# Optimization experiments

Measured on AMD Instinct MI355X. Metric: run time of the kernel, lower is better.

The kernel has to match this reference:

```python
import jax, jax.numpy as jnp
import numpy as np

H = 1024      # hidden_dim
NH = 16       # num_heads
HD = H // NH  # head_dim
FF = 4 * H
EPS = 1e-5

def _ln(x, g, b):
    m = jnp.mean(x, axis=-1, keepdims=True)
    v = jnp.var(x, axis=-1, keepdims=True)
    return (x - m) * jax.lax.rsqrt(v + EPS) * g + b

def setup_inputs() -> dict:
    key = jax.random.key(0)
    ks = jax.random.split(key, 12)
    s = 1.0 / np.sqrt(H)
    inp = {
        'x': jax.random.normal(ks[0], (2, 2048, H), dtype=jnp.float32),
        'Wq': jax.random.normal(ks[1], (H, H), dtype=jnp.float32) * s,
        'bq': jnp.zeros((H,), dtype=jnp.float32),
        'Wk': jax.random.normal(ks[2], (H, H), dtype=jnp.float32) * s,
        'bk': jnp.zeros((H,), dtype=jnp.float32),
        'Wv': jax.random.normal(ks[3], (H, H), dtype=jnp.float32) * s,
        'bv': jnp.zeros((H,), dtype=jnp.float32),
        'Wo': jax.random.normal(ks[4], (H, H), dtype=jnp.float32) * s,
        'bo': jnp.zeros((H,), dtype=jnp.float32),
        'g1': jnp.ones((H,), dtype=jnp.float32),
        'b1': jnp.zeros((H,), dtype=jnp.float32),
        'W1': jax.random.normal(ks[5], (H, FF), dtype=jnp.float32) * s,
        'bf1': jnp.zeros((FF,), dtype=jnp.float32),
        'W2': jax.random.normal(ks[6], (FF, H), dtype=jnp.float32) * (1.0 / np.sqrt(FF)),
        'bf2': jnp.zeros((H,), dtype=jnp.float32),
        'g2': jnp.ones((H,), dtype=jnp.float32),
        'b2': jnp.zeros((H,), dtype=jnp.float32),
    }
    return inp

def reference(x, Wq, bq, Wk, bk, Wv, bv, Wo, bo, g1, b1, W1, bf1, W2, bf2, g2, b2):
    B, S, _ = x.shape
    residual = x
    xn = _ln(x, g1, b1)
    # [B,S,H] -> [B,NH,S,HD]
    def split_heads(t):
        return t.reshape(B, S, NH, HD).transpose(0, 2, 1, 3)
    q = split_heads(xn @ Wq + bq)
    k = split_heads(xn @ Wk + bk)
    v = split_heads(xn @ Wv + bv)
    scores = jnp.einsum('bhqd,bhkd->bhqk', q, k) / np.sqrt(HD).astype(np.float32)
    attn = jax.nn.softmax(scores, axis=-1)
    ctx = jnp.einsum('bhqk,bhkd->bhqd', attn, v)
    ctx = ctx.transpose(0, 2, 1, 3).reshape(B, S, H)
    out = ctx @ Wo + bo + residual
    residual = out
    on = _ln(out, g2, b2)
    out = jax.nn.relu(on @ W1 + bf1) @ W2 + bf2 + residual
    return out
```

## Files before the change

kernel.cpp:

```cpp
#include <hip/hip_runtime.h>
#include <hip/hip_bf16.h>

constexpr int HDIM = 1024;
constexpr int NHEAD = 16;
constexpr int FFDIM = 4096;
constexpr int SEQLEN = 2048;
constexpr int NTOK = 4096;

typedef __bf16 bf16x8 __attribute__((ext_vector_type(8)));
typedef float f32x4 __attribute__((ext_vector_type(4)));
typedef short s16x4 __attribute__((ext_vector_type(4)));

union U16x8 {
    s16x4 h[2];
    bf16x8 v;
    int4 raw;
    unsigned u[4];
    short s[8];
};

__device__ __forceinline__ short f2bf(float f) {
    union { float f; unsigned u; } c;
    c.f = f;
    return (short)((c.u + 0x8000u) >> 16);
}

__device__ __forceinline__ unsigned cvtpk(float a, float b) {
    __hip_bfloat162 h = __float22bfloat162_rn(float2{a, b});
    return *reinterpret_cast<unsigned*>(&h);
}

__device__ __forceinline__ float exp2_raw(float x) {
    float r;
    asm("v_exp_f32 %0, %1" : "=v"(r) : "v"(x));
    return r;
}

template <int N>
__device__ __forceinline__ void wait_vmcnt() {
    if constexpr (N == 0) asm volatile("s_waitcnt vmcnt(0)" ::: "memory");
    else if constexpr (N == 3) asm volatile("s_waitcnt vmcnt(3)" ::: "memory");
    else if constexpr (N == 4) asm volatile("s_waitcnt vmcnt(4)" ::: "memory");
    else if constexpr (N == 6) asm volatile("s_waitcnt vmcnt(6)" ::: "memory");
    else static_assert(N == 0, "unsupported vmcnt");
}
__device__ __forceinline__ void barrier_fence() {
    __builtin_amdgcn_s_barrier();
    asm volatile("" ::: "memory");
}

__device__ __forceinline__ void gload16(const void* gsrc, void* lds) {
    __builtin_amdgcn_global_load_lds(
        (const __attribute__((address_space(1))) unsigned int*)gsrc,
        (__attribute__((address_space(3))) unsigned int*)lds, 16, 0, 0);
}


constexpr float QSCALE = 0.18033688011112042f;

__global__ __launch_bounds__(256)
void wconv_all(const float* __restrict__ Wq, const float* __restrict__ Wk,
               const float* __restrict__ Wv, const float* __restrict__ Wo,
               const float* __restrict__ W1, const float* __restrict__ W2,
               short* __restrict__ qkvT, short* __restrict__ WoT,
               short* __restrict__ W1T, short* __restrict__ W2T) {
    int i = blockIdx.x;
    const float* W;
    short* WT;
    int K, N, bx, by;
    if (i < 2048) {
        const int w = i >> 9;
        i &= 511;
        K = HDIM; N = HDIM; bx = i & 3; by = i >> 2;
        W = w == 0 ? Wq : w == 1 ? Wk : w == 2 ? Wv : Wo;
        WT = w == 3 ? WoT : qkvT + (size_t)w * HDIM * HDIM;
    } else if (i < 4096) {
        i -= 2048;
        K = HDIM; N = FFDIM; bx = i & 15; by = i >> 4;
        W = W1; WT = W1T;
    } else {
        i -= 4096;
        K = FFDIM; N = HDIM; bx = i & 3; by = i >> 2;
        W = W2; WT = W2T;
    }
    const int n = bx * 256 + threadIdx.x;
    const int g = by >> 2, fc = by & 3;
    const int k0 = g * 32 + fc * 4;
    float a[4], c[4];
#pragma unroll
    for (int j = 0; j < 4; ++j) a[j] = W[(size_t)(k0 + j) * N + n];
#pragma unroll
    for (int j = 0; j < 4; ++j) c[j] = W[(size_t)(k0 + 16 + j) * N + n];
    U16x8 u;
    u.u[0] = cvtpk(a[0], a[1]);
    u.u[1] = cvtpk(a[2], a[3]);
    u.u[2] = cvtpk(c[0], c[1]);
    u.u[3] = cvtpk(c[2], c[3]);
    *(int4*)(WT + (size_t)n * K + by * 8) = u.raw;
}

__global__ __launch_bounds__(256)
void ln_bf16(const float* __restrict__ x, const float* __restrict__ g,
             const float* __restrict__ b, short* __restrict__ out) {
    const int row = blockIdx.x, t = threadIdx.x;
    const float* xr = x + (size_t)row * HDIM;
    float4 v = *(const float4*)&xr[t * 4];
    float s = v.x + v.y + v.z + v.w;
    float ss = v.x * v.x + v.y * v.y + v.z * v.z + v.w * v.w;
#pragma unroll
    for (int o = 32; o > 0; o >>= 1) {
        s += __shfl_down(s, o);
        ss += __shfl_down(ss, o);
    }
    __shared__ float red[8];
    const int wv = t >> 6, ln = t & 63;
    if (ln == 0) { red[wv] = s; red[4 + wv] = ss; }
    __syncthreads();
    s = red[0] + red[1] + red[2] + red[3];
    ss = red[4] + red[5] + red[6] + red[7];
    const float mean = s * (1.0f / HDIM);
    const float var = ss * (1.0f / HDIM) - mean * mean;
    const float rstd = rsqrtf(var + 1e-5f);
    float4 gv = *(const float4*)&g[t * 4];
    float4 bv = *(const float4*)&b[t * 4];
    union { s16x4 h4; uint2 u2; } pk;
    pk.u2.x = cvtpk((v.x - mean) * rstd * gv.x + bv.x, (v.y - mean) * rstd * gv.y + bv.y);
    pk.u2.y = cvtpk((v.z - mean) * rstd * gv.z + bv.z, (v.w - mean) * rstd * gv.w + bv.w);
    const int kk = (t * 4) & 31;
    const int dst = ((t * 4) & ~31) + ((kk & 15) >> 2) * 8 + (kk >> 4) * 4;
    *(s16x4*)&out[(size_t)row * HDIM + dst] = pk.h4;
}

template <int BM, int BN, int MODE>
__global__ __launch_bounds__(256, ((BM + BN) == 256) ? 3 : 4)
void gemm_bf16(const short* __restrict__ A, const short* __restrict__ BT,
               const float* __restrict__ bias, const float* __restrict__ resid,
               void* __restrict__ outp, int M, int N, int K,
               const float* __restrict__ bias2, const float* __restrict__ bias3,
               void* __restrict__ out3) {
    constexpr int MI = BM / 32, NJ = BN / 32;
    constexpr int NSEG = (BM + BN) / 16;
    constexpr int PW = NSEG / 4;
    constexpr int BUFS = (BM + BN) * 32;
    __shared__ short LdsF[3 * BUFS];
    const int tid = threadIdx.x;
    const int lane = tid & 63, wave = tid >> 6;
    const int wm = wave >> 1, wn = wave & 1;
    const int l15 = lane & 15, lg = lane >> 4;
    const int lsw = lg ^ ((l15 >> 1) & 3);
    const int m0 = blockIdx.x * BM, n0 = blockIdx.y * BN;
    const int nk = K >> 5;
    const int sr = lane >> 2;
    const int sc8 = (((lane & 3) ^ ((sr >> 1) & 3))) * 8;

    auto stage = [&](int buf, int kt) {
#pragma unroll
        for (int p = 0; p < PW; ++p) {
            const int s = wave + p * 4;
            const short* src = (s < BM / 16)
                ? A + (size_t)(m0 + s * 16 + sr) * K + kt * 32 + sc8
                : BT + (size_t)(n0 + (s - BM / 16) * 16 + sr) * K + kt * 32 + sc8;
            const int off = __builtin_amdgcn_readfirstlane(buf * BUFS * 2 + s * 1024);
            gload16(src, (char*)LdsF + off);
        }
    };

    f32x4 acc[MI][NJ] = {};
    stage(0, 0);
    if (nk > 1) stage(1, 1);
    for (int kt = 0; kt < nk; ++kt) {
        const int buf = kt % 3;
        if (kt + 1 < nk) wait_vmcnt<PW>();
        else wait_vmcnt<0>();
        barrier_fence();
        if (kt + 2 < nk) stage((kt + 2) % 3, kt + 2);
        bf16x8 af[MI], bfr[NJ];
#pragma unroll
        for (int i = 0; i < MI; ++i)
            af[i] = *(const bf16x8*)&LdsF[buf * BUFS +
                                          (wm * (BM / 2) + i * 16 + l15) * 32 + lsw * 8];
#pragma unroll
        for (int j = 0; j < NJ; ++j)
            bfr[j] = *(const bf16x8*)&LdsF[buf * BUFS +
                                           (BM + wn * (BN / 2) + j * 16 + l15) * 32 + lsw * 8];
#pragma unroll
        for (int i = 0; i < MI; ++i)
#pragma unroll
            for (int j = 0; j < NJ; ++j)
                acc[i][j] = __builtin_amdgcn_mfma_f32_16x16x32_bf16(af[i], bfr[j], acc[i][j], 0, 0, 0);
    }

    const int rbase = m0 + wm * (BM / 2);
    const int cbase = n0 + wn * (BN / 2);
    if constexpr (MODE == 0) {
#pragma unroll
        for (int i = 0; i < MI; ++i)
#pragma unroll
            for (int j = 0; j < NJ; ++j) {
                const int c = cbase + j * 16 + l15;
                const float bv = bias[c];
#pragma unroll
                for (int ii = 0; ii < 4; ++ii) {
                    const int r = rbase + i * 16 + lg * 4 + ii;
                    const size_t idx = (size_t)r * N + c;
                    ((float*)outp)[idx] = acc[i][j][ii] + bv + resid[idx];
                }
            }
    } else if constexpr (MODE == 1) {
#pragma unroll
        for (int i = 0; i < MI; ++i)
#pragma unroll
            for (int j = 0; j < NJ; ++j) {
                const int c = cbase + j * 16 + l15;
                const float bv = bias[c];
                const int cp = (c & ~31) | ((l15 >> 2) * 8 + (j & 1) * 4 + (l15 & 3));
#pragma unroll
                for (int ii = 0; ii < 4; ++ii) {
                    const int r = rbase + i * 16 + lg * 4 + ii;
                    float v = acc[i][j][ii] + bv;
                    v = v > 0.0f ? v : 0.0f;
                    ((short*)outp)[(size_t)r * N + cp] = f2bf(v);
                }
            }
    } else {
        const int which = n0 >> 10;
        if (which < 2) {
            const float* bb = which == 0 ? bias : bias2;
            const float qs = which == 0 ? QSCALE : 1.0f;
            short* QKp = (short*)outp;
#pragma unroll
            for (int i = 0; i < MI; ++i)
#pragma unroll
                for (int j = 0; j < NJ; ++j) {
                    const int c = cbase + j * 16 + l15;
                    const float bv = bb[c & 1023];
                    const int cp = (c & ~31) | ((l15 >> 2) * 8 + (j & 1) * 4 + (l15 & 3));
#pragma unroll
                    for (int ii = 0; ii < 4; ++ii) {
                        const int r = rbase + i * 16 + lg * 4 + ii;
                        QKp[(size_t)r * 2048 + cp] = f2bf((acc[i][j][ii] + bv) * qs);
                    }
                }
        } else {
            short* VTp = (short*)out3;
#pragma unroll
            for (int j = 0; j < NJ; ++j) {
                const int c = cbase + j * 16 + l15;
                const int cc = c - 2048;
                const int hh = cc >> 6, dd = cc & 63;
                const float bv = bias3[cc];
#pragma unroll
                for (int i = 0; i < MI; ++i) {
                    const int r0 = rbase + i * 16 + lg * 4;
                    const int bb_ = r0 >> 11;
                    const int s0 = r0 & (SEQLEN - 1);
                    const int sbase = (s0 & ~31) + lg * 8 + (i & 1) * 4;
                    union { s16x4 h4; uint2 u2; } pk;
                    pk.u2.x = cvtpk(acc[i][j][0] + bv, acc[i][j][1] + bv);
                    pk.u2.y = cvtpk(acc[i][j][2] + bv, acc[i][j][3] + bv);
                    *(s16x4*)&VTp[(((size_t)(bb_ * NHEAD + hh)) * 64 + dd) * SEQLEN + sbase] = pk.h4;
                }
            }
        }
    }
}

__global__ __launch_bounds__(256, 4)
void attn_fwd(const short* __restrict__ QK, const short* __restrict__ VT,
              short* __restrict__ ctx) {
    __shared__ short KlF[2 * 4096];
    __shared__ short VlF[2 * 4096];
    const int tid = threadIdx.x, lane = tid & 63, wave = tid >> 6;
    const int l15 = lane & 15, lg = lane >> 4;
    const int lsw = lg ^ ((l15 >> 1) & 3);
    const int bid = blockIdx.x;
    const int xcd = bid & 7, li = bid >> 3;
    const int bh = xcd * 4 + (li >> 5);
    const int qt = li & 31;
    const int b = bh >> 4, h = bh & 15;
    const size_t tokbase = (size_t)b * SEQLEN;
    const int sr = lane >> 2;
    const int sc8 = (((lane & 3) ^ ((sr >> 1) & 3))) * 8;

    const short* kp = QK + (tokbase + wave * 16 + sr) * 2048 + 1024 + h * 64 + sc8;
    const short* vp = VT + ((size_t)bh * 64 + wave * 16 + sr) * SEQLEN + sc8;

    auto stage = [&](int buf) {
        const int off = __builtin_amdgcn_readfirstlane(buf * 8192 + wave * 1024);
        gload16(kp, (char*)KlF + off);
        gload16(kp + 32, (char*)KlF + off + 4096);
        gload16(vp, (char*)VlF + off);
        gload16(vp + 32, (char*)VlF + off + 4096);
    };

    const short* qp = QK + (tokbase + qt * 64 + wave * 16 + l15) * 2048 + h * 64;
    bf16x8 qf[2];
    qf[0] = *(const bf16x8*)(qp + lg * 8);
    qf[1] = *(const bf16x8*)(qp + 32 + lg * 8);

    U16x8 uo;
#pragma unroll
    for (int j = 0; j < 8; ++j) uo.s[j] = 0x3F80;
    const bf16x8 onesv = uo.v;

    f32x4 o[4] = {};
    f32x4 Lacc = {};
    stage(0);
    for (int kt = 0; kt < SEQLEN / 64; ++kt) {
        const int buf = kt & 1;
        __syncthreads();
        if (kt + 1 < SEQLEN / 64) {
            kp += 64 * 2048;
            vp += 64;
            stage(buf ^ 1);
        }

        f32x4 sc[4];
        __builtin_amdgcn_s_setprio(1);
#pragma unroll
        for (int j = 0; j < 4; ++j) {
            bf16x8 kf0 = *(const bf16x8*)&KlF[buf * 4096 + (j * 16 + l15) * 32 + lsw * 8];
            bf16x8 kf1 = *(const bf16x8*)&KlF[buf * 4096 + 2048 + (j * 16 + l15) * 32 + lsw * 8];
            f32x4 z = {};
            z = __builtin_amdgcn_mfma_f32_16x16x32_bf16(kf0, qf[0], z, 0, 0, 0);
            sc[j] = __builtin_amdgcn_mfma_f32_16x16x32_bf16(kf1, qf[1], z, 0, 0, 0);
        }
        __builtin_amdgcn_s_setprio(0);

        U16x8 u0, u1;
        u0.u[0] = cvtpk(exp2_raw(sc[0][0]), exp2_raw(sc[0][1]));
        u0.u[1] = cvtpk(exp2_raw(sc[0][2]), exp2_raw(sc[0][3]));
        u0.u[2] = cvtpk(exp2_raw(sc[1][0]), exp2_raw(sc[1][1]));
        u0.u[3] = cvtpk(exp2_raw(sc[1][2]), exp2_raw(sc[1][3]));
        u1.u[0] = cvtpk(exp2_raw(sc[2][0]), exp2_raw(sc[2][1]));
        u1.u[1] = cvtpk(exp2_raw(sc[2][2]), exp2_raw(sc[2][3]));
        u1.u[2] = cvtpk(exp2_raw(sc[3][0]), exp2_raw(sc[3][1]));
        u1.u[3] = cvtpk(exp2_raw(sc[3][2]), exp2_raw(sc[3][3]));

        __builtin_amdgcn_s_setprio(1);
#pragma unroll
        for (int ks = 0; ks < 2; ++ks) {
            const bf16x8 pf = ks == 0 ? u0.v : u1.v;
            Lacc = __builtin_amdgcn_mfma_f32_16x16x32_bf16(onesv, pf, Lacc, 0, 0, 0);
#pragma unroll
            for (int fd = 0; fd < 4; ++fd) {
                bf16x8 vf = *(const bf16x8*)&VlF[buf * 4096 + ks * 2048 + (fd * 16 + l15) * 32 + lsw * 8];
                o[fd] = __builtin_amdgcn_mfma_f32_16x16x32_bf16(vf, pf, o[fd], 0, 0, 0);
            }
        }
        __builtin_amdgcn_s_setprio(0);
    }

    const float rl = 1.0f / Lacc[0];
    const int qrow = qt * 64 + wave * 16 + l15;
    short* crow = ctx + (tokbase + qrow) * HDIM + h * 64;
#pragma unroll
    for (int fd = 0; fd < 4; ++fd) {
        s16x4 v4;
#pragma unroll
        for (int ii = 0; ii < 4; ++ii) v4[ii] = f2bf(o[fd][ii] * rl);
        *(s16x4*)(crow + (fd >> 1) * 32 + lg * 8 + (fd & 1) * 4) = v4;
    }
}

extern "C" void kernel_launch(void* const* d_in, const int* in_sizes, int n_in,
                              void* d_out, int out_size, void* d_ws, size_t ws_size,
                              hipStream_t stream) {
    const float* x  = (const float*)d_in[0];
    const float* Wq = (const float*)d_in[1];
    const float* bq = (const float*)d_in[2];
    const float* Wk = (const float*)d_in[3];
    const float* bk = (const float*)d_in[4];
    const float* Wv = (const float*)d_in[5];
    const float* bv = (const float*)d_in[6];
    const float* Wo = (const float*)d_in[7];
    const float* bo = (const float*)d_in[8];
    const float* g1 = (const float*)d_in[9];
    const float* b1 = (const float*)d_in[10];
    const float* W1 = (const float*)d_in[11];
    const float* bf1 = (const float*)d_in[12];
    const float* W2 = (const float*)d_in[13];
    const float* bf2 = (const float*)d_in[14];
    const float* g2 = (const float*)d_in[15];
    const float* b2 = (const float*)d_in[16];

    char* ws = (char*)d_ws;
    const size_t MB = 1024 * 1024;
    short* qkvT = (short*)(ws + 0 * MB);
    short* WoT  = (short*)(ws + 6 * MB);
    short* W1T  = (short*)(ws + 8 * MB);
    short* W2T  = (short*)(ws + 16 * MB);
    short* xn   = (short*)(ws + 24 * MB);
    short* QKb  = (short*)(ws + 32 * MB);
    short* VTb  = (short*)(ws + 48 * MB);
    short* ctx  = (short*)(ws + 56 * MB);
    float* out1 = (float*)(ws + 64 * MB);
    short* h1   = (short*)(ws + 32 * MB);

    wconv_all<<<6144, 256, 0, stream>>>(Wq, Wk, Wv, Wo, W1, W2, qkvT, WoT, W1T, W2T);

    ln_bf16<<<NTOK, 256, 0, stream>>>(x, g1, b1, xn);

    gemm_bf16<128, 128, 2><<<dim3(NTOK / 128, 3072 / 128), 256, 0, stream>>>(
        xn, qkvT, bq, nullptr, QKb, NTOK, 3072, HDIM, bk, bv, VTb);

    attn_fwd<<<1024, 256, 0, stream>>>(QKb, VTb, ctx);

    gemm_bf16<128, 64, 0><<<dim3(NTOK / 128, HDIM / 64), 256, 0, stream>>>(
        ctx, WoT, bo, x, out1, NTOK, HDIM, HDIM, nullptr, nullptr, nullptr);

    ln_bf16<<<NTOK, 256, 0, stream>>>(out1, g2, b2, xn);

    gemm_bf16<128, 128, 1><<<dim3(NTOK / 128, FFDIM / 128), 256, 0, stream>>>(
        xn, W1T, bf1, nullptr, h1, NTOK, FFDIM, HDIM, nullptr, nullptr, nullptr);

    gemm_bf16<128, 64, 0><<<dim3(NTOK / 128, HDIM / 64), 256, 0, stream>>>(
        h1, W2T, bf2, out1, (float*)d_out, NTOK, HDIM, FFDIM, nullptr, nullptr, nullptr);
}
```

Before: 229.0 us.

## Split GEMM pipelining: double-buffer 128x128, paired k-tile 6-buffer pipeline for 128x64

Adds a PIPE template parameter to the bf16 GEMM. The 128x128 GEMMs (QKV, FFN1) drop from a 3-stage LDS ring to a plain 2-buffer scheme with __syncthreads, which uses less shared memory per block. The 128x64 GEMMs (Wo, FFN2) move to a 6-buffer pipeline that loads and computes two k-tiles per barrier, with launch bounds lowered to 2 blocks/SM. The aim is to cut barrier count and improve latency hiding on the narrow GEMMs, at the cost of occupancy, and with exposed load latency on the double-buffered ones.

```diff
diff --git a/kernel.cpp b/kernel.cpp
--- a/kernel.cpp
+++ b/kernel.cpp
@@ -39,10 +39,8 @@
 template <int N>
 __device__ __forceinline__ void wait_vmcnt() {
     if constexpr (N == 0) asm volatile("s_waitcnt vmcnt(0)" ::: "memory");
-    else if constexpr (N == 3) asm volatile("s_waitcnt vmcnt(3)" ::: "memory");
-    else if constexpr (N == 4) asm volatile("s_waitcnt vmcnt(4)" ::: "memory");
     else if constexpr (N == 6) asm volatile("s_waitcnt vmcnt(6)" ::: "memory");
-    else static_assert(N == 0, "unsupported vmcnt");
+    else static_assert(N == 0 || N == 6, "unsupported vmcnt");
 }
 __device__ __forceinline__ void barrier_fence() {
     __builtin_amdgcn_s_barrier();
@@ -131,8 +129,8 @@
     *(s16x4*)&out[(size_t)row * HDIM + dst] = pk.h4;
 }
 
-template <int BM, int BN, int MODE>
-__global__ __launch_bounds__(256, ((BM + BN) == 256) ? 3 : 4)
+template <int BM, int BN, int MODE, int PIPE>
+__global__ __launch_bounds__(256, PIPE ? 2 : (((BM + BN) == 256) ? 3 : 4))
 void gemm_bf16(const short* __restrict__ A, const short* __restrict__ BT,
                const float* __restrict__ bias, const float* __restrict__ resid,
                void* __restrict__ outp, int M, int N, int K,
@@ -142,7 +140,9 @@
     constexpr int NSEG = (BM + BN) / 16;
     constexpr int PW = NSEG / 4;
     constexpr int BUFS = (BM + BN) * 32;
-    __shared__ short LdsF[3 * BUFS];
+    constexpr int NBUF = PIPE ? 6 : 2;
+    static_assert(!PIPE || (BM + BN) == 192, "PIPE=1 tuned for PW=3 (vmcnt 6)");
+    __shared__ short LdsF[NBUF * BUFS];
     const int tid = threadIdx.x;
     const int lane = tid & 63, wave = tid >> 6;
     const int wm = wave >> 1, wn = wave & 1;
@@ -164,16 +164,7 @@
             gload16(src, (char*)LdsF + off);
         }
     };
-
-    f32x4 acc[MI][NJ] = {};
-    stage(0, 0);
-    if (nk > 1) stage(1, 1);
-    for (int kt = 0; kt < nk; ++kt) {
-        const int buf = kt % 3;
-        if (kt + 1 < nk) wait_vmcnt<PW>();
-        else wait_vmcnt<0>();
-        barrier_fence();
-        if (kt + 2 < nk) stage((kt + 2) % 3, kt + 2);
+    auto compute = [&](int buf, f32x4 (&acc)[MI][NJ]) {
         bf16x8 af[MI], bfr[NJ];
 #pragma unroll
         for (int i = 0; i < MI; ++i)
@@ -188,6 +179,34 @@
 #pragma unroll
             for (int j = 0; j < NJ; ++j)
                 acc[i][j] = __builtin_amdgcn_mfma_f32_16x16x32_bf16(af[i], bfr[j], acc[i][j], 0, 0, 0);
+    };
+
+    f32x4 acc[MI][NJ] = {};
+    if constexpr (PIPE == 0) {
+        stage(0, 0);
+        for (int kt = 0; kt < nk; ++kt) {
+            const int buf = kt & 1;
+            __syncthreads();
+            if (kt + 1 < nk) stage(buf ^ 1, kt + 1);
+            compute(buf, acc);
+        }
+    } else {
+        stage(0, 0); stage(1, 1); stage(2, 2); stage(3, 3);
+        const int np = nk >> 1;
+        int pc = 0, ps = 2;
+        for (int t = 0; t < np; ++t) {
+            if (t + 1 < np) wait_vmcnt<6>();
+            else wait_vmcnt<0>();
+            barrier_fence();
+            if (t + 2 < np) {
+                stage(ps * 2, 2 * t + 4);
+                stage(ps * 2 + 1, 2 * t + 5);
+            }
+            compute(pc * 2, acc);
+            compute(pc * 2 + 1, acc);
+            pc = (pc == 2) ? 0 : pc + 1;
+            ps = (ps == 2) ? 0 : ps + 1;
+        }
     }
 
     const int rbase = m0 + wm * (BM / 2);
@@ -401,19 +420,19 @@
 
     ln_bf16<<<NTOK, 256, 0, stream>>>(x, g1, b1, xn);
 
-    gemm_bf16<128, 128, 2><<<dim3(NTOK / 128, 3072 / 128), 256, 0, stream>>>(
+    gemm_bf16<128, 128, 2, 0><<<dim3(NTOK / 128, 3072 / 128), 256, 0, stream>>>(
         xn, qkvT, bq, nullptr, QKb, NTOK, 3072, HDIM, bk, bv, VTb);
 
     attn_fwd<<<1024, 256, 0, stream>>>(QKb, VTb, ctx);
 
-    gemm_bf16<128, 64, 0><<<dim3(NTOK / 128, HDIM / 64), 256, 0, stream>>>(
+    gemm_bf16<128, 64, 0, 1><<<dim3(NTOK / 128, HDIM / 64), 256, 0, stream>>>(
         ctx, WoT, bo, x, out1, NTOK, HDIM, HDIM, nullptr, nullptr, nullptr);
 
     ln_bf16<<<NTOK, 256, 0, stream>>>(out1, g2, b2, xn);
 
-    gemm_bf16<128, 128, 1><<<dim3(NTOK / 128, FFDIM / 128), 256, 0, stream>>>(
+    gemm_bf16<128, 128, 1, 0><<<dim3(NTOK / 128, FFDIM / 128), 256, 0, stream>>>(
         xn, W1T, bf1, nullptr, h1, NTOK, FFDIM, HDIM, nullptr, nullptr, nullptr);
 
-    gemm_bf16<128, 64, 0><<<dim3(NTOK / 128, HDIM / 64), 256, 0, stream>>>(
+    gemm_bf16<128, 64, 0, 1><<<dim3(NTOK / 128, HDIM / 64), 256, 0, stream>>>(
         h1, W2T, bf2, out1, (float*)d_out, NTOK, HDIM, FFDIM, nullptr, nullptr, nullptr);
 }
```

Result: faster. 222.2 us (-3.0%).
